# Kernel optimization log

Measured on AMD Instinct MI355X. Metric: run time of the kernel, lower is better.

## Reference

```python
import jax, jax.numpy as jnp
import numpy as np

TAB_DIM = 6
C = 64
B, X, Y, Z = 2, 64, 64, 64
EPS = float(np.finfo(np.float32).eps)


def _gauss_1d(mu, sigma, size):
    # mu, sigma: (B, C) -> mask (B, C, size)
    coords = jnp.arange(size, dtype=jnp.float32)  # (size,)
    mu = mu * (size / 2.0) + (size / 2.0) - 0.5
    sigma = sigma * 3.5 + EPS
    d = (coords[None, None, :] - mu[:, :, None]) / sigma[:, :, None]
    return jnp.exp(-0.5 * d * d)


def _frob(t):
    return jnp.sqrt(jnp.sum(t * t))


def setup_inputs() -> dict:
    key = jax.random.key(0)
    ks = jax.random.split(key, 10)
    h = C // 2
    def lin(k, fan_in, fan_out):
        bound = 1.0 / np.sqrt(fan_in)
        kw, kb = jax.random.split(k)
        w = jax.random.uniform(kw, (fan_out, fan_in), jnp.float32, -bound, bound)
        b = jax.random.uniform(kb, (fan_out,), jnp.float32, -bound, bound)
        return w, b
    w1, b1 = lin(ks[0], TAB_DIM, h)
    w2, b2 = lin(ks[1], h, h)
    wp, bp = lin(ks[2], h, 5 * C)
    ws, bs = lin(ks[3], h, 3 * C)
    x = jax.random.normal(ks[4], (B, C, X, Y, Z), jnp.float32)
    tab = jax.random.normal(ks[5], (B, TAB_DIM), jnp.float32)
    return {"x": x, "tab": tab, "w1": w1, "b1": b1, "w2": w2, "b2": b2,
            "wp": wp, "bp": bp, "ws": ws, "bs": bs}


def reference(x, tab, w1, b1, w2, b2, wp, bp, ws, bs):
    # hypernetwork (tiny MLPs)
    emb = jnp.tanh(tab @ w1.T + b1)
    emb = jnp.tanh(emb @ w2.T + b2)
    p = emb @ wp.T + bp                     # (B, 5C)
    s = jax.nn.sigmoid(emb @ ws.T + bs)     # (B, 3C)
    scale = p[..., :C]
    shift = p[..., C:2 * C]
    mu_a = jnp.tanh(p[..., 2 * C:3 * C])
    mu_b = jnp.tanh(p[..., 3 * C:4 * C])
    mu_c = jnp.tanh(p[..., 4 * C:])
    sigma_a = s[..., :C]
    sigma_b = s[..., C:2 * C]
    sigma_c = s[..., 2 * C:]

    l2 = _frob(scale) + _frob(shift) + _frob(sigma_a) + _frob(sigma_b) + _frob(sigma_c)

    _, _, sx, sy, sz = x.shape
    gx = _gauss_1d(mu_a, sigma_a, sx)  # (B, C, X)
    gy = _gauss_1d(mu_b, sigma_b, sy)  # (B, C, Y)
    gz = _gauss_1d(mu_c, sigma_c, sz)  # (B, C, Z)

    # rank-1 outer product over X,Y,Z == the chained matmuls in torch
    a = gx[:, :, :, None, None] * gy[:, :, None, :, None] * gz[:, :, None, None, :]

    out = (1.0 - scale)[:, :, None, None, None] * x * a + shift[:, :, None, None, None]
    return out, l2
```

## Files before the change

### kernel.cpp

```cpp
#include <hip/hip_runtime.h>
#include <math.h>

#define EPSF 1.1920929e-07f

typedef float f4 __attribute__((ext_vector_type(4)));

__device__ __forceinline__ float sigmoidf_(float v) { return 1.0f / (1.0f + expf(-v)); }

__global__ void __launch_bounds__(256) fused_kernel(
        const float* __restrict__ xin, const float* __restrict__ tab,
        const float* __restrict__ w1,  const float* __restrict__ b1,
        const float* __restrict__ w2,  const float* __restrict__ b2,
        const float* __restrict__ wp,  const float* __restrict__ bp,
        const float* __restrict__ wsg, const float* __restrict__ bsg,
        float* __restrict__ out, int out_last)
{
    __shared__ float emb1[2][32];
    __shared__ float emb2[2][32];
    __shared__ float head[8];
    __shared__ float gys[64];
    __shared__ f4    gz4[16];
    __shared__ float pv_sh, sh_sh;

    const int blk = blockIdx.x;
    const int bc  = blk >> 6;
    const int xi  = blk & 63;
    const int b   = bc >> 6;
    const int c   = bc & 63;
    const int tid = threadIdx.x;

    if (tid < 64) {
        int bb = tid >> 5, j = tid & 31;
        float acc = b1[j];
        #pragma unroll
        for (int k = 0; k < 6; ++k) acc += tab[bb * 6 + k] * w1[j * 6 + k];
        emb1[bb][j] = tanhf(acc);
    }
    __syncthreads();

    if (tid < 64) {
        int bb = tid >> 5, j = tid & 31;
        float acc = b2[j];
        #pragma unroll
        for (int k = 0; k < 32; ++k) acc += emb1[bb][k] * w2[j * 32 + k];
        emb2[bb][j] = tanhf(acc);
    }
    __syncthreads();

    if (tid < 8) {
        const float* W  = (tid < 5) ? wp  : wsg;
        const float* Bv = (tid < 5) ? bp  : bsg;
        int row = ((tid < 5) ? tid : (tid - 5)) * 64 + c;
        float acc = Bv[row];
        #pragma unroll
        for (int k = 0; k < 32; ++k) acc += emb2[b][k] * W[row * 32 + k];
        head[tid] = acc;
    }
    __syncthreads();

    if (tid < 64) {
        float m  = tanhf(head[3]) * 32.0f + 31.5f;
        float sg = sigmoidf_(head[6]) * 3.5f + EPSF;
        float d  = ((float)tid - m) / sg;
        gys[tid] = expf(-0.5f * d * d);
    } else if (tid < 128) {
        int i = tid - 64;
        float m  = tanhf(head[4]) * 32.0f + 31.5f;
        float sg = sigmoidf_(head[7]) * 3.5f + EPSF;
        float d  = ((float)i - m) / sg;
        ((float*)gz4)[i] = expf(-0.5f * d * d);
    } else if (tid == 128) {
        float m  = tanhf(head[2]) * 32.0f + 31.5f;
        float sg = sigmoidf_(head[5]) * 3.5f + EPSF;
        float d  = ((float)xi - m) / sg;
        pv_sh = (1.0f - head[0]) * expf(-0.5f * d * d);
        sh_sh = head[1];
    }

    if (blk == 0) {
        __shared__ float sq[5][128];
        for (int t = tid; t < 640; t += 256) {
            int q = t / 128, r = t % 128;
            int bb = r >> 6, cc = r & 63;
            const float* W  = (q < 2) ? wp  : wsg;
            const float* Bv = (q < 2) ? bp  : bsg;
            int row = ((q < 2) ? q : (q - 2)) * 64 + cc;
            float acc = Bv[row];
            #pragma unroll
            for (int k = 0; k < 32; ++k) acc += emb2[bb][k] * W[row * 32 + k];
            if (q >= 2) acc = sigmoidf_(acc);
            sq[q][r] = acc * acc;
        }
        __syncthreads();
        if (tid == 0) {
            float tot = 0.0f;
            for (int q = 0; q < 5; ++q) {
                float ssum = 0.0f;
                for (int i = 0; i < 128; ++i) ssum += sq[q][i];
                tot += sqrtf(ssum);
            }
            out[out_last] = tot;
        }
    }
    __syncthreads();

    const float pv = pv_sh;
    const float sh = sh_sh;
    const int   yb = tid >> 4;
    const f4    vz = gz4[tid & 15];
    const f4 w0 = vz * (pv * gys[yb]);
    const f4 w1_ = vz * (pv * gys[yb + 16]);
    const f4 w2_ = vz * (pv * gys[yb + 32]);
    const f4 w3_ = vz * (pv * gys[yb + 48]);
    const f4 shv = {sh, sh, sh, sh};

    const f4* x4 = (const f4*)(xin + (size_t)blk * 4096);
    f4*       o4 = (f4*)(out + (size_t)blk * 4096);

    f4 x0 = __builtin_nontemporal_load(&x4[tid]);
    f4 x1 = __builtin_nontemporal_load(&x4[tid + 256]);
    f4 x2 = __builtin_nontemporal_load(&x4[tid + 512]);
    f4 x3 = __builtin_nontemporal_load(&x4[tid + 768]);

    __builtin_nontemporal_store(w0  * x0 + shv, &o4[tid]);
    __builtin_nontemporal_store(w1_ * x1 + shv, &o4[tid + 256]);
    __builtin_nontemporal_store(w2_ * x2 + shv, &o4[tid + 512]);
    __builtin_nontemporal_store(w3_ * x3 + shv, &o4[tid + 768]);
}

extern "C" void kernel_launch(void* const* d_in, const int* in_sizes, int n_in,
                              void* d_out, int out_size, void* d_ws, size_t ws_size,
                              hipStream_t stream)
{
    const float* x   = (const float*)d_in[0];
    const float* tab = (const float*)d_in[1];
    const float* w1  = (const float*)d_in[2];
    const float* b1  = (const float*)d_in[3];
    const float* w2  = (const float*)d_in[4];
    const float* b2  = (const float*)d_in[5];
    const float* wp  = (const float*)d_in[6];
    const float* bp  = (const float*)d_in[7];
    const float* wsg = (const float*)d_in[8];
    const float* bsg = (const float*)d_in[9];

    float* out = (float*)d_out;

    fused_kernel<<<2 * 64 * 64, 256, 0, stream>>>(
        x, tab, w1, b1, w2, b2, wp, bp, wsg, bsg, out, out_size - 1);
}
```

Before: 49.62 us.

## Issue x loads before hypernetwork prologue and use fast transcendental math

Moves the four nontemporal x loads to the top of the kernel so global memory latency overlaps the serial per-block MLP prologue and its barriers. It also replaces tanhf/expf/sigmoid with __expf-based fast versions and vectorises the weight reads as float4. Holding the loaded x values through the prologue raises register pressure, and the fast math slightly changes numerical accuracy.

```diff
diff --git a/kernel.cpp b/kernel.cpp
--- a/kernel.cpp
+++ b/kernel.cpp
@@ -5,7 +5,19 @@
 
 typedef float f4 __attribute__((ext_vector_type(4)));
 
-__device__ __forceinline__ float sigmoidf_(float v) { return 1.0f / (1.0f + expf(-v)); }
+__device__ __forceinline__ float sigmoid_fast(float v) {
+    return 1.0f / (1.0f + __expf(-v));
+}
+__device__ __forceinline__ float tanh_fast(float x) {
+    float ax = fabsf(x);
+    float e  = __expf(-2.0f * ax);
+    float t  = (1.0f - e) / (1.0f + e);
+    return copysignf(t, x);
+}
+__device__ __forceinline__ float gauss_fast(float i, float m, float sg) {
+    float d = (i - m) / sg;
+    return __expf(-0.5f * d * d);
+}
 
 __global__ void __launch_bounds__(256) fused_kernel(
         const float* __restrict__ xin, const float* __restrict__ tab,
@@ -29,21 +41,33 @@
     const int c   = bc & 63;
     const int tid = threadIdx.x;
 
+    const f4* x4 = (const f4*)(xin + (size_t)blk * 4096);
+    f4*       o4 = (f4*)(out + (size_t)blk * 4096);
+    f4 x0 = __builtin_nontemporal_load(&x4[tid]);
+    f4 x1 = __builtin_nontemporal_load(&x4[tid + 256]);
+    f4 x2 = __builtin_nontemporal_load(&x4[tid + 512]);
+    f4 x3 = __builtin_nontemporal_load(&x4[tid + 768]);
+
     if (tid < 64) {
         int bb = tid >> 5, j = tid & 31;
         float acc = b1[j];
         #pragma unroll
         for (int k = 0; k < 6; ++k) acc += tab[bb * 6 + k] * w1[j * 6 + k];
-        emb1[bb][j] = tanhf(acc);
+        emb1[bb][j] = tanh_fast(acc);
     }
     __syncthreads();
 
     if (tid < 64) {
         int bb = tid >> 5, j = tid & 31;
+        const f4* wr = (const f4*)(w2 + j * 32);
         float acc = b2[j];
         #pragma unroll
-        for (int k = 0; k < 32; ++k) acc += emb1[bb][k] * w2[j * 32 + k];
-        emb2[bb][j] = tanhf(acc);
+        for (int q = 0; q < 8; ++q) {
+            f4 wv = wr[q];
+            acc += wv.x * emb1[bb][q * 4 + 0] + wv.y * emb1[bb][q * 4 + 1]
+                 + wv.z * emb1[bb][q * 4 + 2] + wv.w * emb1[bb][q * 4 + 3];
+        }
+        emb2[bb][j] = tanh_fast(acc);
     }
     __syncthreads();
 
@@ -51,29 +75,31 @@
         const float* W  = (tid < 5) ? wp  : wsg;
         const float* Bv = (tid < 5) ? bp  : bsg;
         int row = ((tid < 5) ? tid : (tid - 5)) * 64 + c;
+        const f4* wr = (const f4*)(W + row * 32);
         float acc = Bv[row];
         #pragma unroll
-        for (int k = 0; k < 32; ++k) acc += emb2[b][k] * W[row * 32 + k];
+        for (int q = 0; q < 8; ++q) {
+            f4 wv = wr[q];
+            acc += wv.x * emb2[b][q * 4 + 0] + wv.y * emb2[b][q * 4 + 1]
+                 + wv.z * emb2[b][q * 4 + 2] + wv.w * emb2[b][q * 4 + 3];
+        }
         head[tid] = acc;
     }
     __syncthreads();
 
     if (tid < 64) {
-        float m  = tanhf(head[3]) * 32.0f + 31.5f;
-        float sg = sigmoidf_(head[6]) * 3.5f + EPSF;
-        float d  = ((float)tid - m) / sg;
-        gys[tid] = expf(-0.5f * d * d);
+        float m  = tanh_fast(head[3]) * 32.0f + 31.5f;
+        float sg = sigmoid_fast(head[6]) * 3.5f + EPSF;
+        gys[tid] = gauss_fast((float)tid, m, sg);
     } else if (tid < 128) {
         int i = tid - 64;
-        float m  = tanhf(head[4]) * 32.0f + 31.5f;
-        float sg = sigmoidf_(head[7]) * 3.5f + EPSF;
-        float d  = ((float)i - m) / sg;
-        ((float*)gz4)[i] = expf(-0.5f * d * d);
+        float m  = tanh_fast(head[4]) * 32.0f + 31.5f;
+        float sg = sigmoid_fast(head[7]) * 3.5f + EPSF;
+        ((float*)gz4)[i] = gauss_fast((float)i, m, sg);
     } else if (tid == 128) {
-        float m  = tanhf(head[2]) * 32.0f + 31.5f;
-        float sg = sigmoidf_(head[5]) * 3.5f + EPSF;
-        float d  = ((float)xi - m) / sg;
-        pv_sh = (1.0f - head[0]) * expf(-0.5f * d * d);
+        float m  = tanh_fast(head[2]) * 32.0f + 31.5f;
+        float sg = sigmoid_fast(head[5]) * 3.5f + EPSF;
+        pv_sh = (1.0f - head[0]) * gauss_fast((float)xi, m, sg);
         sh_sh = head[1];
     }
 
@@ -85,10 +111,15 @@
             const float* W  = (q < 2) ? wp  : wsg;
             const float* Bv = (q < 2) ? bp  : bsg;
             int row = ((q < 2) ? q : (q - 2)) * 64 + cc;
+            const f4* wr = (const f4*)(W + row * 32);
             float acc = Bv[row];
             #pragma unroll
-            for (int k = 0; k < 32; ++k) acc += emb2[bb][k] * W[row * 32 + k];
-            if (q >= 2) acc = sigmoidf_(acc);
+            for (int u = 0; u < 8; ++u) {
+                f4 wv = wr[u];
+                acc += wv.x * emb2[bb][u * 4 + 0] + wv.y * emb2[bb][u * 4 + 1]
+                     + wv.z * emb2[bb][u * 4 + 2] + wv.w * emb2[bb][u * 4 + 3];
+            }
+            if (q >= 2) acc = sigmoid_fast(acc);
             sq[q][r] = acc * acc;
         }
         __syncthreads();
@@ -108,24 +139,16 @@
     const float sh = sh_sh;
     const int   yb = tid >> 4;
     const f4    vz = gz4[tid & 15];
-    const f4 w0 = vz * (pv * gys[yb]);
-    const f4 w1_ = vz * (pv * gys[yb + 16]);
-    const f4 w2_ = vz * (pv * gys[yb + 32]);
-    const f4 w3_ = vz * (pv * gys[yb + 48]);
+    const float s0 = pv * gys[yb];
+    const float s1 = pv * gys[yb + 16];
+    const float s2 = pv * gys[yb + 32];
+    const float s3 = pv * gys[yb + 48];
     const f4 shv = {sh, sh, sh, sh};
 
-    const f4* x4 = (const f4*)(xin + (size_t)blk * 4096);
-    f4*       o4 = (f4*)(out + (size_t)blk * 4096);
-
-    f4 x0 = __builtin_nontemporal_load(&x4[tid]);
-    f4 x1 = __builtin_nontemporal_load(&x4[tid + 256]);
-    f4 x2 = __builtin_nontemporal_load(&x4[tid + 512]);
-    f4 x3 = __builtin_nontemporal_load(&x4[tid + 768]);
-
-    __builtin_nontemporal_store(w0  * x0 + shv, &o4[tid]);
-    __builtin_nontemporal_store(w1_ * x1 + shv, &o4[tid + 256]);
-    __builtin_nontemporal_store(w2_ * x2 + shv, &o4[tid + 512]);
-    __builtin_nontemporal_store(w3_ * x3 + shv, &o4[tid + 768]);
+    __builtin_nontemporal_store((vz * x0) * s0 + shv, &o4[tid]);
+    __builtin_nontemporal_store((vz * x1) * s1 + shv, &o4[tid + 256]);
+    __builtin_nontemporal_store((vz * x2) * s2 + shv, &o4[tid + 512]);
+    __builtin_nontemporal_store((vz * x3) * s3 + shv, &o4[tid + 768]);
 }
 
 extern "C" void kernel_launch(void* const* d_in, const int* in_sizes, int n_in,
```

Measured after the change: 52.29 us. +5.4%, slower.
